# Optimization experiments

Hardware: AMD Instinct MI355X
Metric: run time of the kernel (lower is better)

The kernel has to match this reference:

```python
import jax, jax.numpy as jnp
import numpy as np

B, L, C, H = 32, 641, 768, 12
MEM = 128  # memory slots K; state token at index K; tokens are causal after that


def _block_mask(L, K):
    # rows i attend to cols j per FusedAttention:
    #  memory rows (i<K): attend to memory+state (j<=K)
    #  state row (i==K): attends to everything
    #  token rows (i>K): attend to memory+state (j<=K) and causally to tokens (K<j<=i)
    i = jnp.arange(L)[:, None]
    j = jnp.arange(L)[None, :]
    mem_rows = (i < K) & (j <= K)
    state_row = (i == K)
    tok_rows = (i > K) & ((j <= K) | ((j > K) & (j <= i)))
    return mem_rows | state_row | tok_rows  # (L, L) bool


def setup_inputs() -> dict:
    key = jax.random.key(0)
    k1, k2, k3 = jax.random.split(key, 3)
    x = jax.random.normal(k1, (B, L, C), dtype=jnp.float32)
    W_attn = jax.random.normal(k2, (C, 3 * C), dtype=jnp.float32) * 0.02
    W_proj = jax.random.normal(k3, (C, C), dtype=jnp.float32) * 0.02
    return {"x": x, "W_attn": W_attn, "W_proj": W_proj, "mem_size": MEM}


def reference(x, W_attn, W_proj, mem_size):
    Bb, Ll, Cc = x.shape
    hd = Cc // H
    qkv = x @ W_attn  # (B, L, 3C)
    q, k, v = jnp.split(qkv, 3, axis=-1)
    # (B, H, L, hd)
    q = q.reshape(Bb, Ll, H, hd).transpose(0, 2, 1, 3)
    k = k.reshape(Bb, Ll, H, hd).transpose(0, 2, 1, 3)
    v = v.reshape(Bb, Ll, H, hd).transpose(0, 2, 1, 3)
    mask = _block_mask(Ll, mem_size)  # (L, L)
    scale = 1.0 / jnp.sqrt(jnp.asarray(hd, dtype=x.dtype))
    att = jnp.einsum("bhqd,bhkd->bhqk", q, k) * scale
    att = jnp.where(mask[None, None, :, :], att, jnp.asarray(-jnp.inf, att.dtype))
    att = jax.nn.softmax(att, axis=-1)
    y = jnp.einsum("bhqk,bhkd->bhqd", att, v)
    y = y.transpose(0, 2, 1, 3).reshape(Bb, Ll, Cc)
    return y @ W_proj
```

## Files before the change

kernel.cpp:

```cpp
#include <hip/hip_runtime.h>
#include <stdint.h>

#define B_SZ 32
#define L_SZ 641
#define C_SZ 768
#define H_SZ 12
#define HD 64
#define MEMK 128
#define M_REAL (B_SZ * L_SZ)
#define M_PAD 20608
#define N_QKV (3 * C_SZ)
#define NQP 6
#define QK_STRIDE 1536
#define VT_STRIDE 648
#define SCL_LOG2E 0.18033688f
#define FIXED_MAX 8.0f

typedef __attribute__((ext_vector_type(8))) short short8;
typedef __attribute__((ext_vector_type(4))) float f32x4;
typedef __attribute__((ext_vector_type(4))) unsigned short ushort4v;

__device__ inline unsigned short f2bf(float x) {
  union { float f; uint32_t u; } v; v.f = x;
  uint32_t r = v.u + 0x7fffu + ((v.u >> 16) & 1u);
  return (unsigned short)(r >> 16);
}
__device__ inline float bf2f(short v) {
  union { float f; uint32_t u; } x; x.u = ((uint32_t)(unsigned short)v) << 16;
  return x.f;
}

__device__ inline void gload_lds16(const void* g, void* l) {
  __builtin_amdgcn_global_load_lds(
      (const __attribute__((address_space(1))) uint32_t*)g,
      (__attribute__((address_space(3))) uint32_t*)l, 16, 0, 0);
}

__global__ __launch_bounds__(256) void k_conv_x(const float* __restrict__ src,
                                                unsigned short* __restrict__ dst,
                                                int n4) {
  int i = blockIdx.x * 256 + threadIdx.x;
  if (i >= n4) return;
  float4 v = *(const float4*)(src + (size_t)i * 4);
  ushort4v o = { f2bf(v.x), f2bf(v.y), f2bf(v.z), f2bf(v.w) };
  *(ushort4v*)(dst + (size_t)i * 4) = o;
}

__global__ __launch_bounds__(256) void k_transpose_bf16(const float* __restrict__ src,
                                                        unsigned short* __restrict__ dst,
                                                        int R, int Ccol,
                                                        float scale, int scale_cmax) {
  __shared__ float tile[32][33];
  int c0 = blockIdx.x * 32, r0 = blockIdx.y * 32;
  int tx = threadIdx.x & 31, ty = threadIdx.x >> 5;
  for (int i = ty; i < 32; i += 8)
    tile[i][tx] = src[(size_t)(r0 + i) * Ccol + c0 + tx];
  __syncthreads();
  float sc = (c0 < scale_cmax) ? scale : 1.0f;
  for (int i = ty; i < 32; i += 8)
    dst[(size_t)(c0 + i) * R + r0 + tx] = f2bf(tile[tx][i] * sc);
}

template <int MODE>
__global__ __launch_bounds__(256) void k_gemm(const short* __restrict__ A,
                                              const short* __restrict__ Bt,
                                              void* __restrict__ Cp,
                                              short* __restrict__ vt,
                                              int Mreal, int N, int K) {
  __shared__ short As[2][128 * 64];
  __shared__ short Bs[2][128 * 64];
  int nwg = gridDim.x;
  int qq = nwg >> 3, rr = nwg & 7;
  int x8 = blockIdx.x & 7, i8 = blockIdx.x >> 3;
  int wg = (x8 < rr ? x8 * (qq + 1) : rr * (qq + 1) + (x8 - rr) * qq) + i8;
  const int tiles_n = N >> 7;
  int tm = wg / tiles_n, tn = wg % tiles_n;
  int m0 = tm << 7, n0 = tn << 7;
  int lane = threadIdx.x & 63, wave = threadIdx.x >> 6;
  int wr = wave >> 1, wc = wave & 1;
  int l15 = lane & 15, g = lane >> 4;

  f32x4 acc[4][4];
  f32x4 z = {0.f, 0.f, 0.f, 0.f};
#pragma unroll
  for (int i = 0; i < 4; ++i)
#pragma unroll
    for (int j = 0; j < 4; ++j) acc[i][j] = z;

  int arow = lane >> 3;
  int acol = (lane & 7) * 8;

#define STAGE(K0, BUF)                                                        \
  {                                                                           \
    _Pragma("unroll")                                                         \
    for (int cc = 0; cc < 4; ++cc) {                                          \
      int rb = (cc * 4 + wave) * 8;                                           \
      gload_lds16(A + (size_t)(m0 + rb + arow) * K + ((K0) + acol),           \
                  (char*)As[BUF] + rb * 128);                                 \
      gload_lds16(Bt + (size_t)(n0 + rb + arow) * K + ((K0) + acol),          \
                  (char*)Bs[BUF] + rb * 128);                                 \
    }                                                                         \
  }

  STAGE(0, 0);
  STAGE(64, 1);
  int nk = K >> 6;
  for (int t = 0; t < nk; ++t) {
    int buf = t & 1;
    if (t + 1 < nk) {
      asm volatile("s_waitcnt vmcnt(8)" ::: "memory");
    } else {
      asm volatile("s_waitcnt vmcnt(0)" ::: "memory");
    }
    __builtin_amdgcn_s_barrier();
#pragma unroll
    for (int ks = 0; ks < 2; ++ks) {
      short8 a[4], b[4];
      if (MODE == 3) {
#pragma unroll
        for (int nf = 0; nf < 4; ++nf)
          a[nf] = *(const short8*)&Bs[buf][(wr * 64 + nf * 16 + l15) * 64 + ks * 32 + g * 8];
#pragma unroll
        for (int mf = 0; mf < 4; ++mf)
          b[mf] = *(const short8*)&As[buf][(wc * 64 + mf * 16 + l15) * 64 + ks * 32 + g * 8];
      } else {
#pragma unroll
        for (int mf = 0; mf < 4; ++mf)
          a[mf] = *(const short8*)&As[buf][(wr * 64 + mf * 16 + l15) * 64 + ks * 32 + g * 8];
#pragma unroll
        for (int nf = 0; nf < 4; ++nf)
          b[nf] = *(const short8*)&Bs[buf][(wc * 64 + nf * 16 + l15) * 64 + ks * 32 + g * 8];
      }
#pragma unroll
      for (int i = 0; i < 4; ++i)
#pragma unroll
        for (int j = 0; j < 4; ++j)
          acc[i][j] = __builtin_amdgcn_mfma_f32_16x16x32_bf16(a[i], b[j], acc[i][j], 0, 0, 0);
    }
    __builtin_amdgcn_s_barrier();
    __builtin_amdgcn_sched_barrier(0);
    if (t + 2 < nk) STAGE((t + 2) << 6, buf);
  }
#undef STAGE

  if (MODE == 3) {
#pragma unroll
    for (int nf = 0; nf < 4; ++nf) {
#pragma unroll
      for (int reg = 0; reg < 4; ++reg) {
        int n = n0 + wr * 64 + nf * 16 + g * 4 + reg;
        int h = n >> 6, d = n & 63;
        int xr = (d & 7) << 3;
#pragma unroll
        for (int mf = 0; mf < 4; ++mf) {
          int m = m0 + wc * 64 + mf * 16 + l15;
          if (m >= Mreal) continue;
          int bb = (unsigned)m / 641u;
          int key = m - bb * 641;
          int k2 = (key >= 640) ? key : (key ^ xr);
          vt[((size_t)(bb * H_SZ + h) * HD + d) * VT_STRIDE + k2] = f2bf(acc[nf][mf][reg]);
        }
      }
    }
    return;
  }
#pragma unroll
  for (int mf = 0; mf < 4; ++mf) {
#pragma unroll
    for (int reg = 0; reg < 4; ++reg) {
      int m = m0 + wr * 64 + mf * 16 + g * 4 + reg;
      if (m >= Mreal) continue;
      int xr = 0;
      if (MODE == 2) {
        int bb = (unsigned)m / 641u;
        int key = m - bb * 641;
        xr = (key & 7) << 3;
      }
#pragma unroll
      for (int nf = 0; nf < 4; ++nf) {
        int n = n0 + wc * 64 + nf * 16 + l15;
        float v = acc[mf][nf][reg];
        if (MODE == 2) {
          int nn = (n >= C_SZ) ? (n ^ xr) : n;
          ((unsigned short*)Cp)[(size_t)m * QK_STRIDE + nn] = f2bf(v);
        } else
          ((float*)Cp)[(size_t)m * N + n] = v;
      }
    }
  }
}

__global__ __launch_bounds__(512) void k_attn(const short* __restrict__ qk,
                                              const short* __restrict__ vt,
                                              short* __restrict__ y) {
  __shared__ short Ks[2][64 * 64];
  __shared__ short Vt[2][64 * 64];
  __shared__ short Ps[8][16 * 64];

  int bid = blockIdx.x;
  int work = (bid & 7) * 288 + (bid >> 3);
  int qp = work % NQP;
  int rem = work / NQP;
  int h = rem % H_SZ;
  int b = rem / H_SZ;
  int q0 = qp * 128;
  int tid = threadIdx.x;
  int lane = tid & 63, w = tid >> 6;
  int wgp = w >> 2;
  int l15 = lane & 15, g = lane >> 4;
  int q0w = q0 + wgp * 64 + (w & 3) * 16;

  size_t qbase = (size_t)(b * L_SZ + q0w + l15) * QK_STRIDE + h * HD;
  short8 qa[2];
#pragma unroll
  for (int ks = 0; ks < 2; ++ks)
    qa[ks] = *(const short8*)&qk[qbase + ks * 32 + g * 8];

  f32x4 o[4];
  float l_run[4];
  f32x4 z = {0.f, 0.f, 0.f, 0.f};
  f32x4 m8 = {-FIXED_MAX, -FIXED_MAX, -FIXED_MAX, -FIXED_MAX};
#pragma unroll
  for (int df = 0; df < 4; ++df) o[df] = z;
#pragma unroll
  for (int r = 0; r < 4; ++r) l_run[r] = 0.f;

  int jmax[4];
#pragma unroll
  for (int reg = 0; reg < 4; ++reg) {
    int i = q0w + g * 4 + reg;
    jmax[reg] = (i == MEMK) ? (L_SZ - 1) : (i < MEMK ? MEMK : i);
  }
  int jm_min = (q0w <= MEMK) ? MEMK : q0w;

  int q1 = q0 + 127; if (q1 > L_SZ - 1) q1 = L_SZ - 1;
  int col_max = (q0 <= MEMK && MEMK <= q1) ? (L_SZ - 1) : (q1 < MEMK ? MEMK : q1);
  int qw1 = q0w + 15;
  bool dead = (q0w >= L_SZ);
  int wcol = (q0w <= MEMK && MEMK <= qw1) ? (L_SZ - 1) : (qw1 < MEMK ? MEMK : qw1);
  if (dead) wcol = -1;

  size_t kbase = (size_t)b * L_SZ * QK_STRIDE + C_SZ + h * HD;
  size_t vbase = (size_t)(b * H_SZ + h) * HD * VT_STRIDE;

  int i0 = tid >> 3, j0e = (tid & 7) * 8;
  int rswz = (l15 & 7) << 4;

#define STAGE_ATTN(C0, BUF)                                                   \
  {                                                                           \
    gload_lds16(qk + kbase + (size_t)((C0) + i0) * QK_STRIDE + j0e,           \
                (char*)Ks[BUF] + w * 1024);                                   \
    gload_lds16(vt + vbase + (size_t)i0 * VT_STRIDE + (C0) + j0e,             \
                (char*)Vt[BUF] + w * 1024);                                   \
  }

  STAGE_ATTN(0, 0);

  int nt = col_max >> 6;
  for (int t = 0; t <= nt; ++t) {
    int c0 = t << 6;
    int buf = t & 1;
    __syncthreads();
    if (t < nt) STAGE_ATTN(c0 + 64, buf ^ 1);
    if (c0 > wcol) continue;
    int vswz = (c0 >= 640) ? 0 : rswz;

    f32x4 s[4];
#pragma unroll
    for (int kf = 0; kf < 4; ++kf) {
      f32x4 sa = m8;
#pragma unroll
      for (int ks = 0; ks < 2; ++ks) {
        short8 kb = *(const short8*)((char*)Ks[buf] +
                        (kf * 16 + l15) * 128 + ((ks * 64 + g * 16) ^ rswz));
        sa = __builtin_amdgcn_mfma_f32_16x16x32_bf16(qa[ks], kb, sa, 0, 0, 0);
      }
      s[kf] = sa;
    }

    if (c0 + 63 > jm_min) {
#pragma unroll
      for (int kf = 0; kf < 4; ++kf) {
        int j = c0 + kf * 16 + l15;
#pragma unroll
        for (int reg = 0; reg < 4; ++reg)
          s[kf][reg] = (j <= jmax[reg]) ? s[kf][reg] : -1e30f;
      }
    }

#pragma unroll
    for (int kf = 0; kf < 4; ++kf)
#pragma unroll
      for (int reg = 0; reg < 4; ++reg)
        s[kf][reg] = exp2f(s[kf][reg]);
#pragma unroll
    for (int reg = 0; reg < 4; ++reg)
      l_run[reg] += (s[0][reg] + s[1][reg]) + (s[2][reg] + s[3][reg]);

#pragma unroll
    for (int reg = 0; reg < 4; ++reg) {
      int q = g * 4 + reg;
      char* prow = (char*)Ps[w] + q * 128;
      int qswz = (q & 7) << 4;
#pragma unroll
      for (int kf = 0; kf < 4; kf += 2) {
        uint32_t r;
        asm("v_cvt_pk_bf16_f32 %0, %1, %2"
            : "=v"(r) : "v"(s[kf][reg]), "v"(s[kf + 1][reg]));
        *(short*)(prow + ((kf * 32 + l15 * 2) ^ qswz)) = (short)(r & 0xffff);
        *(short*)(prow + (((kf + 1) * 32 + l15 * 2) ^ qswz)) = (short)(r >> 16);
      }
    }

    short8 pa[2];
#pragma unroll
    for (int ks = 0; ks < 2; ++ks)
      pa[ks] = *(const short8*)((char*)Ps[w] + l15 * 128 + ((ks * 64 + g * 16) ^ rswz));
#pragma unroll
    for (int df = 0; df < 4; ++df) {
#pragma unroll
      for (int ks = 0; ks < 2; ++ks) {
        short8 vb = *(const short8*)((char*)Vt[buf] +
                        (df * 16 + l15) * 128 + ((ks * 64 + g * 16) ^ vswz));
        o[df] = __builtin_amdgcn_mfma_f32_16x16x32_bf16(pa[ks], vb, o[df], 0, 0, 0);
      }
    }
  }
#undef STAGE_ATTN

#pragma unroll
  for (int reg = 0; reg < 4; ++reg) {
    float ls = l_run[reg];
    ls += __shfl_xor(ls, 1);
    ls += __shfl_xor(ls, 2);
    ls += __shfl_xor(ls, 4);
    ls += __shfl_xor(ls, 8);
    int i = q0w + g * 4 + reg;
    if (i >= L_SZ) continue;
    float inv = 1.0f / ls;
#pragma unroll
    for (int df = 0; df < 4; ++df)
      y[(size_t)(b * L_SZ + i) * C_SZ + h * HD + df * 16 + l15] = (short)f2bf(o[df][reg] * inv);
  }
}

extern "C" void kernel_launch(void* const* d_in, const int* in_sizes, int n_in,
                              void* d_out, int out_size, void* d_ws, size_t ws_size,
                              hipStream_t stream) {
  const float* x = (const float*)d_in[0];
  const float* Wa = (const float*)d_in[1];
  const float* Wp = (const float*)d_in[2];
  float* out = (float*)d_out;

  char* ws = (char*)d_ws;
  size_t off0 = 0;
  short* x_bf = (short*)(ws + off0);
  size_t off1 = off0 + (size_t)M_PAD * C_SZ * 2;
  short* Wa_t = (short*)(ws + off1);
  size_t off2 = off1 + (size_t)N_QKV * C_SZ * 2;
  short* Wp_t = (short*)(ws + off2);
  size_t off3 = off2 + (size_t)C_SZ * C_SZ * 2;
  short* qk = (short*)(ws + off3);
  size_t off4 = off3 + (size_t)M_REAL * QK_STRIDE * 2;
  short* vt = (short*)(ws + off4);
  size_t need = off4 + (size_t)B_SZ * H_SZ * HD * VT_STRIDE * 2 + 4096;
  if (ws_size < need) return;

  int n4 = M_REAL * C_SZ / 4;
  k_conv_x<<<(n4 + 255) / 256, 256, 0, stream>>>(x, (unsigned short*)x_bf, n4);
  k_transpose_bf16<<<dim3(N_QKV / 32, C_SZ / 32), 256, 0, stream>>>(
      Wa, (unsigned short*)Wa_t, C_SZ, N_QKV, SCL_LOG2E, C_SZ);
  k_transpose_bf16<<<dim3(C_SZ / 32, C_SZ / 32), 256, 0, stream>>>(
      Wp, (unsigned short*)Wp_t, C_SZ, C_SZ, 1.0f, 0);

  k_gemm<2><<<(M_PAD / 128) * (QK_STRIDE / 128), 256, 0, stream>>>(
      x_bf, Wa_t, (void*)qk, nullptr, M_REAL, QK_STRIDE, C_SZ);
  k_gemm<3><<<(M_PAD / 128) * (C_SZ / 128), 256, 0, stream>>>(
      x_bf, Wa_t + (size_t)QK_STRIDE * C_SZ, nullptr, vt, M_REAL, C_SZ, C_SZ);
  k_attn<<<B_SZ * H_SZ * NQP, 512, 0, stream>>>(qk, vt, x_bf );
  k_gemm<0><<<(M_PAD / 128) * (C_SZ / 128), 256, 0, stream>>>(
      x_bf, Wp_t, (void*)out, nullptr, M_REAL, C_SZ, C_SZ);
}
```

Baseline: 259.1 us.

## Pre-swizzle GEMM operands in global memory to avoid LDS bank conflicts

Producers of the GEMM operands (x conversion, weight transposes, attention output) now write rows with an XOR swizzle of 16-byte chunks keyed by the row index. The GEMM's direct global-to-LDS loads therefore land already swizzled, and the LDS fragment reads apply the matching XOR to cut bank conflicts on the MFMA operand loads. This adds some index arithmetic to the producers and couples every producer's layout to the GEMM's reader, so any producer that is missed gives wrong results.

```diff
diff --git a/kernel.cpp b/kernel.cpp
--- a/kernel.cpp
+++ b/kernel.cpp
@@ -43,7 +43,10 @@
   if (i >= n4) return;
   float4 v = *(const float4*)(src + (size_t)i * 4);
   ushort4v o = { f2bf(v.x), f2bf(v.y), f2bf(v.z), f2bf(v.w) };
-  *(ushort4v*)(dst + (size_t)i * 4) = o;
+  int m = (unsigned)i / 192u;
+  int k = (i - m * 192) * 4;
+  int kk = k ^ ((m & 7) << 3);
+  *(ushort4v*)(dst + (size_t)m * C_SZ + kk) = o;
 }
 
 __global__ __launch_bounds__(256) void k_transpose_bf16(const float* __restrict__ src,
@@ -57,8 +60,11 @@
     tile[i][tx] = src[(size_t)(r0 + i) * Ccol + c0 + tx];
   __syncthreads();
   float sc = (c0 < scale_cmax) ? scale : 1.0f;
-  for (int i = ty; i < 32; i += 8)
-    dst[(size_t)(c0 + i) * R + r0 + tx] = f2bf(tile[tx][i] * sc);
+  for (int i = ty; i < 32; i += 8) {
+    int c = c0 + i;
+    int r = (r0 + tx) ^ ((c & 7) << 3);
+    dst[(size_t)c * R + r] = f2bf(tile[tx][i] * sc);
+  }
 }
 
 template <int MODE>
@@ -79,6 +85,7 @@
   int lane = threadIdx.x & 63, wave = threadIdx.x >> 6;
   int wr = wave >> 1, wc = wave & 1;
   int l15 = lane & 15, g = lane >> 4;
+  int gswz = (l15 & 7) << 4;
 
   f32x4 acc[4][4];
   f32x4 z = {0.f, 0.f, 0.f, 0.f};
@@ -116,20 +123,25 @@
 #pragma unroll
     for (int ks = 0; ks < 2; ++ks) {
       short8 a[4], b[4];
+      int roff = (ks * 64) ^ gswz;
       if (MODE == 3) {
 #pragma unroll
         for (int nf = 0; nf < 4; ++nf)
-          a[nf] = *(const short8*)&Bs[buf][(wr * 64 + nf * 16 + l15) * 64 + ks * 32 + g * 8];
+          a[nf] = *(const short8*)((char*)Bs[buf] +
+                      (wr * 64 + nf * 16 + l15) * 128 + (roff ^ (g * 16)));
 #pragma unroll
         for (int mf = 0; mf < 4; ++mf)
-          b[mf] = *(const short8*)&As[buf][(wc * 64 + mf * 16 + l15) * 64 + ks * 32 + g * 8];
+          b[mf] = *(const short8*)((char*)As[buf] +
+                      (wc * 64 + mf * 16 + l15) * 128 + (roff ^ (g * 16)));
       } else {
 #pragma unroll
         for (int mf = 0; mf < 4; ++mf)
-          a[mf] = *(const short8*)&As[buf][(wr * 64 + mf * 16 + l15) * 64 + ks * 32 + g * 8];
+          a[mf] = *(const short8*)((char*)As[buf] +
+                      (wr * 64 + mf * 16 + l15) * 128 + (roff ^ (g * 16)));
 #pragma unroll
         for (int nf = 0; nf < 4; ++nf)
-          b[nf] = *(const short8*)&Bs[buf][(wc * 64 + nf * 16 + l15) * 64 + ks * 32 + g * 8];
+          b[nf] = *(const short8*)((char*)Bs[buf] +
+                      (wc * 64 + nf * 16 + l15) * 128 + (roff ^ (g * 16)));
       }
 #pragma unroll
       for (int i = 0; i < 4; ++i)
@@ -338,9 +350,13 @@
     int i = q0w + g * 4 + reg;
     if (i >= L_SZ) continue;
     float inv = 1.0f / ls;
-#pragma unroll
-    for (int df = 0; df < 4; ++df)
-      y[(size_t)(b * L_SZ + i) * C_SZ + h * HD + df * 16 + l15] = (short)f2bf(o[df][reg] * inv);
+    size_t m = (size_t)(b * L_SZ + i);
+    int ixr = ((int)(m & 7)) << 3;
+#pragma unroll
+    for (int df = 0; df < 4; ++df) {
+      int col = (df * 16 + l15) ^ ixr;
+      y[m * C_SZ + h * HD + col] = (short)f2bf(o[df][reg] * inv);
+    }
   }
 }
 
```

After: 243.1 us. 1.07x faster.
